# Kernel optimization log

Hardware: AMD Instinct MI355X
Metric: run time of the kernel (lower is better)

The kernel has to match this reference:

```python
import jax, jax.numpy as jnp
import numpy as np


def _pairwise_l2(set1, set2):
    # set1: [B, N, C], set2: [B, M, C] -> [B, N, M] Euclidean distances.
    # Equivalent to ||a - b||_2 computed via the expanded quadratic form,
    # avoiding the O(B*N*M*C) broadcasted-difference intermediate.
    sq1 = jnp.sum(set1 * set1, axis=-1)  # [B, N]
    sq2 = jnp.sum(set2 * set2, axis=-1)  # [B, M]
    inner = jnp.einsum('bnc,bmc->bnm', set1, set2)  # [B, N, M]
    d2 = sq1[:, :, None] + sq2[:, None, :] - 2.0 * inner
    return jnp.sqrt(jnp.maximum(d2, 0.0))


def reference(set1, set2):
    # mode == Hausdorff.average
    if set1.ndim == 2:
        set1 = set1[None]
    if set2.ndim == 2:
        set2 = set2[None]
    distances = _pairwise_l2(set1, set2)  # [B, N, M]
    term_1 = jnp.mean(jnp.min(distances, axis=2), axis=1)  # [B]
    term_2 = jnp.mean(jnp.min(distances, axis=1), axis=1)  # [B]
    res = term_1 + term_2
    if res.shape[0] == 1:
        res = jnp.squeeze(res, axis=0)
    return res


def setup_inputs() -> dict:
    key = jax.random.key(0)
    k1, k2 = jax.random.split(key)
    B, N, M, C = 8, 4096, 4096, 128
    set1 = jax.random.normal(k1, (B, N, C), dtype=jnp.float32)
    set2 = jax.random.normal(k2, (B, M, C), dtype=jnp.float32)
    return {"set1": set1, "set2": set2}
```

## Files before the change

### kernel.cpp

```cpp
#include <hip/hip_runtime.h>

#define B_ 8
#define N_ 4096
#define M_ 4096
#define C_ 128
#define BN_ (B_ * N_)
#define BM_ (B_ * M_)

typedef __attribute__((ext_vector_type(8))) short bf16x8;
typedef __attribute__((ext_vector_type(4))) float floatx4;
typedef __attribute__((ext_vector_type(8))) unsigned short ushort8;

__device__ __forceinline__ unsigned short f2bf(float x) {
    unsigned int u = __float_as_uint(x);
    u += 0x7FFFu + ((u >> 16) & 1u);
    return (unsigned short)(u >> 16);
}

__device__ __forceinline__ void gl2lds16(const void* g, void* l) {
    __builtin_amdgcn_global_load_lds(
        (const __attribute__((address_space(1))) void*)g,
        (__attribute__((address_space(3))) void*)l, 16, 0, 0);
}

__global__ __launch_bounds__(256) void prep_kernel(
    const float* __restrict__ S1, const float* __restrict__ S2,
    float* __restrict__ norms, unsigned short* __restrict__ bfA,
    unsigned short* __restrict__ bfB, float* __restrict__ out) {
    const int lane = threadIdx.x & 63;
    const int w    = threadIdx.x >> 6;
    const int gw   = blockIdx.x * 4 + w;
    const int r4   = lane >> 4;
    const int g4   = lane & 15;
    const int row  = gw * 4 + r4;

    const float* src = (row < BN_) ? S1 + (size_t)row * C_
                                   : S2 + (size_t)(row - BN_) * C_;
    float4 v0 = ((const float4*)src)[g4 * 2];
    float4 v1 = ((const float4*)src)[g4 * 2 + 1];

    float s = v0.x*v0.x + v0.y*v0.y + v0.z*v0.z + v0.w*v0.w
            + v1.x*v1.x + v1.y*v1.y + v1.z*v1.z + v1.w*v1.w;
    s += __shfl_xor(s, 1, 64);
    s += __shfl_xor(s, 2, 64);
    s += __shfl_xor(s, 4, 64);
    s += __shfl_xor(s, 8, 64);

    ushort8 o;
    o[0] = f2bf(v0.x); o[1] = f2bf(v0.y); o[2] = f2bf(v0.z); o[3] = f2bf(v0.w);
    o[4] = f2bf(v1.x); o[5] = f2bf(v1.y); o[6] = f2bf(v1.z); o[7] = f2bf(v1.w);

    unsigned short* dst = (row < BN_) ? bfA + (size_t)row * C_
                                      : bfB + (size_t)(row - BN_) * C_;
    *(ushort8*)&dst[(g4 ^ (row & 15)) * 8] = o;

    if (g4 == 0) norms[row] = -0.5f * s;
    if (blockIdx.x == 0 && threadIdx.x < B_) out[threadIdx.x] = 0.f;
}

__global__ __launch_bounds__(256, 2) void hausdorff_mfma(
    const unsigned short* __restrict__ Abf, const unsigned short* __restrict__ Bbf,
    const float* __restrict__ ahalf_g, const float* __restrict__ bhalf_g,
    float* __restrict__ rowpart, float* __restrict__ colpart) {

    __shared__ unsigned short B_lds[2][64 * 128];
    __shared__ float colmax_lds[2][1024];

    const int b     = blockIdx.z;
    const int row0  = blockIdx.x * 128;
    const int panel = blockIdx.y;
    const int tid   = threadIdx.x;
    const int lane  = tid & 63;
    const int w     = tid >> 6;
    const int lm    = lane & 15;
    const int quad  = lane >> 4;
    const int wrow  = (w >> 1) * 64;
    const int qc    = (w & 1) * 32;
    const int rh    = w >> 1;
    const int ch    = w & 1;

    const unsigned short* Aws = Abf + ((size_t)b * N_ + row0) * C_;
    const unsigned short* Bws = Bbf + ((size_t)b * M_ + (size_t)panel * 1024) * C_;
    const float* bhalf = bhalf_g + (size_t)b * M_ + panel * 1024;

    #pragma unroll
    for (int k = 0; k < 4; ++k) {
        const int off = w * 2048 + k * 512;
        gl2lds16(Aws + off + lane * 8,        &B_lds[0][off]);
        gl2lds16(Aws + 8192 + off + lane * 8, &B_lds[1][off]);
    }

    float ha[16];
    #pragma unroll
    for (int i = 0; i < 4; ++i) {
        float4 t = *(const float4*)&ahalf_g[(size_t)b * N_ + row0 + wrow + 16 * i + 4 * quad];
        ha[4*i+0] = t.x; ha[4*i+1] = t.y; ha[4*i+2] = t.z; ha[4*i+3] = t.w;
    }

    float rv[16];
    #pragma unroll
    for (int v = 0; v < 16; ++v) rv[v] = -1e30f;

    __syncthreads();

    bf16x8 af[4][4];
    {
        const unsigned short* Abuf = &B_lds[w >> 1][0];
        #pragma unroll
        for (int i = 0; i < 4; ++i)
            #pragma unroll
            for (int c = 0; c < 4; ++c)
                af[i][c] = *(const bf16x8*)
                    &Abuf[(16 * i + lm) * 128 + (((c * 4 + quad) ^ lm) * 8)];
    }

    __syncthreads();

    #pragma unroll
    for (int k = 0; k < 4; ++k) {
        const int off = w * 2048 + k * 512;
        gl2lds16(Bws + off + lane * 8, &B_lds[0][off]);
    }

    for (int it = 0; it < 16; ++it) {
        const int cur = it & 1;
        __syncthreads();

        if (it < 15) {
            const unsigned short* Bt = Bws + (size_t)(it + 1) * 64 * C_;
            #pragma unroll
            for (int k = 0; k < 4; ++k) {
                const int off = w * 2048 + k * 512;
                gl2lds16(Bt + off + lane * 8, &B_lds[cur ^ 1][off]);
            }
        }
        const float hb0 = bhalf[it * 64 + qc + lm];
        const float hb1 = bhalf[it * 64 + qc + 16 + lm];

        bf16x8 bf[2][4];
        #pragma unroll
        for (int j = 0; j < 2; ++j)
            #pragma unroll
            for (int c = 0; c < 4; ++c)
                bf[j][c] = *(const bf16x8*)
                    &B_lds[cur][(qc + 16 * j + lm) * 128 + (((c * 4 + quad) ^ lm) * 8)];

        floatx4 acc[4][2];
        #pragma unroll
        for (int i = 0; i < 4; ++i)
            #pragma unroll
            for (int r = 0; r < 4; ++r) {
                acc[i][0][r] = ha[4 * i + r] + hb0;
                acc[i][1][r] = ha[4 * i + r] + hb1;
            }
        #pragma unroll
        for (int c = 0; c < 4; ++c)
            #pragma unroll
            for (int i = 0; i < 4; ++i)
                #pragma unroll
                for (int j = 0; j < 2; ++j)
                    acc[i][j] = __builtin_amdgcn_mfma_f32_16x16x32_bf16(
                        af[i][c], bf[j][c], acc[i][j], 0, 0, 0);

        float cv0a = -1e30f, cv0b = -1e30f, cv1a = -1e30f, cv1b = -1e30f;
        #pragma unroll
        for (int i = 0; i < 4; ++i) {
            #pragma unroll
            for (int r = 0; r < 4; ++r)
                rv[4 * i + r] = fmaxf(rv[4 * i + r],
                                      fmaxf(acc[i][0][r], acc[i][1][r]));
            float m0 = fmaxf(fmaxf(acc[i][0][0], acc[i][0][1]),
                             fmaxf(acc[i][0][2], acc[i][0][3]));
            float m1 = fmaxf(fmaxf(acc[i][1][0], acc[i][1][1]),
                             fmaxf(acc[i][1][2], acc[i][1][3]));
            if (i & 1) { cv0b = fmaxf(cv0b, m0); cv1b = fmaxf(cv1b, m1); }
            else       { cv0a = fmaxf(cv0a, m0); cv1a = fmaxf(cv1a, m1); }
        }
        float cv0 = fmaxf(cv0a, cv0b), cv1 = fmaxf(cv1a, cv1b);
        cv0 = fmaxf(cv0, __shfl_xor(cv0, 16, 64));
        cv0 = fmaxf(cv0, __shfl_xor(cv0, 32, 64));
        cv1 = fmaxf(cv1, __shfl_xor(cv1, 16, 64));
        cv1 = fmaxf(cv1, __shfl_xor(cv1, 32, 64));
        if (quad == 0) {
            const int c0 = it * 64 + qc + lm;
            colmax_lds[rh][c0]      = cv0;
            colmax_lds[rh][c0 + 16] = cv1;
        }
    }

    float* rowmax_lds = (float*)&B_lds[0][0];
    #pragma unroll
    for (int s = 1; s < 16; s <<= 1)
        #pragma unroll
        for (int v = 0; v < 16; ++v)
            rv[v] = fmaxf(rv[v], __shfl_xor(rv[v], s, 64));
    if (lm == 0) {
        #pragma unroll
        for (int v = 0; v < 16; ++v)
            rowmax_lds[ch * 128 + wrow + 16 * (v >> 2) + 4 * quad + (v & 3)] = rv[v];
    }

    __syncthreads();

    #pragma unroll
    for (int k = 0; k < 4; ++k) {
        const int c = tid + 256 * k;
        colpart[((size_t)blockIdx.x * B_ + b) * M_ + (size_t)panel * 1024 + c] =
            fmaxf(colmax_lds[0][c], colmax_lds[1][c]);
    }
    if (tid < 128)
        rowpart[((size_t)panel * B_ + b) * N_ + row0 + tid] =
            fmaxf(rowmax_lds[tid], rowmax_lds[128 + tid]);
}

__global__ __launch_bounds__(256) void hausdorff_reduce(
    const float* __restrict__ rowpart, const float* __restrict__ colpart,
    float* __restrict__ out) {
    __shared__ float ws4[4];
    const int b    = blockIdx.x >> 3;
    const int part = blockIdx.x & 7;
    const int base = part * 512;
    float s = 0.f;
    for (int i = base + (int)threadIdx.x; i < base + 512; i += 256) {
        float ra = fmaxf(rowpart[((size_t)0 * B_ + b) * N_ + i],
                         rowpart[((size_t)1 * B_ + b) * N_ + i]);
        float rb = fmaxf(rowpart[((size_t)2 * B_ + b) * N_ + i],
                         rowpart[((size_t)3 * B_ + b) * N_ + i]);
        float rm = fmaxf(ra, rb);
        float ca = -1e30f, cb = -1e30f;
        #pragma unroll
        for (int x = 0; x < 32; x += 2) {
            ca = fmaxf(ca, colpart[((size_t)x * B_ + b) * M_ + i]);
            cb = fmaxf(cb, colpart[((size_t)(x + 1) * B_ + b) * M_ + i]);
        }
        float cm = fmaxf(ca, cb);
        s += sqrtf(fmaxf(-2.f * rm, 0.f)) * (1.f / N_)
           + sqrtf(fmaxf(-2.f * cm, 0.f)) * (1.f / M_);
    }
    #pragma unroll
    for (int off = 32; off > 0; off >>= 1) s += __shfl_down(s, off, 64);
    if ((threadIdx.x & 63) == 0) ws4[threadIdx.x >> 6] = s;
    __syncthreads();
    if (threadIdx.x == 0)
        atomicAdd(&out[b], ws4[0] + ws4[1] + ws4[2] + ws4[3]);
}

extern "C" void kernel_launch(void* const* d_in, const int* in_sizes, int n_in,
                              void* d_out, int out_size, void* d_ws, size_t ws_size,
                              hipStream_t stream) {
    const float* s1 = (const float*)d_in[0];
    const float* s2 = (const float*)d_in[1];
    float* out = (float*)d_out;

    float* norms         = (float*)d_ws;
    unsigned short* bfA  = (unsigned short*)(norms + BN_ + BM_);
    unsigned short* bfB  = bfA + (size_t)BN_ * C_;
    float* rowpart       = (float*)(bfB + (size_t)BM_ * C_);
    float* colpart       = rowpart + (size_t)4 * B_ * N_;

    prep_kernel<<<(BN_ + BM_) / 16, 256, 0, stream>>>(
        s1, s2, norms, bfA, bfB, out);

    dim3 grid(N_ / 128, M_ / 1024, B_);
    hausdorff_mfma<<<grid, 256, 0, stream>>>(
        bfA, bfB, norms, norms + BN_, rowpart, colpart);

    hausdorff_reduce<<<B_ * 8, 256, 0, stream>>>(rowpart, colpart, out);
}
```

Measured before the change: 123.7 us.

## Enlarge block row tile to 256 so each wave covers all 64 columns

Each block now handles 256 rows of set1, with each wave owning 64 rows and all 64 columns of every B tile, instead of a 2x2 split over 128 rows. A fragments are loaded straight from global memory into registers, bypassing LDS and two barriers. Row maxima are written directly to global memory. This halves the grid and the number of column-partial slabs the reduce kernel reads. The aim is more MFMA work per B tile loaded into LDS and less staging overhead, at the cost of 16 accumulators per wave (more register pressure) and half as many blocks.

```diff
diff --git a/kernel.cpp b/kernel.cpp
--- a/kernel.cpp
+++ b/kernel.cpp
@@ -64,31 +64,30 @@
     float* __restrict__ rowpart, float* __restrict__ colpart) {
 
     __shared__ unsigned short B_lds[2][64 * 128];
-    __shared__ float colmax_lds[2][1024];
+    __shared__ float colmax_lds[4][1024];
 
     const int b     = blockIdx.z;
-    const int row0  = blockIdx.x * 128;
+    const int x     = blockIdx.x;
     const int panel = blockIdx.y;
+    const int row0  = x * 256;
     const int tid   = threadIdx.x;
     const int lane  = tid & 63;
     const int w     = tid >> 6;
     const int lm    = lane & 15;
     const int quad  = lane >> 4;
-    const int wrow  = (w >> 1) * 64;
-    const int qc    = (w & 1) * 32;
-    const int rh    = w >> 1;
-    const int ch    = w & 1;
-
-    const unsigned short* Aws = Abf + ((size_t)b * N_ + row0) * C_;
+    const int wrow  = w * 64;
+
+    const unsigned short* Aws = Abf + ((size_t)b * N_ + row0 + wrow) * C_;
     const unsigned short* Bws = Bbf + ((size_t)b * M_ + (size_t)panel * 1024) * C_;
     const float* bhalf = bhalf_g + (size_t)b * M_ + panel * 1024;
 
-    #pragma unroll
-    for (int k = 0; k < 4; ++k) {
-        const int off = w * 2048 + k * 512;
-        gl2lds16(Aws + off + lane * 8,        &B_lds[0][off]);
-        gl2lds16(Aws + 8192 + off + lane * 8, &B_lds[1][off]);
-    }
+    bf16x8 af[4][4];
+    #pragma unroll
+    for (int i = 0; i < 4; ++i)
+        #pragma unroll
+        for (int c = 0; c < 4; ++c)
+            af[i][c] = *(const bf16x8*)
+                &Aws[(16 * i + lm) * 128 + (((c * 4 + quad) ^ lm) * 8)];
 
     float ha[16];
     #pragma unroll
@@ -100,21 +99,6 @@
     float rv[16];
     #pragma unroll
     for (int v = 0; v < 16; ++v) rv[v] = -1e30f;
-
-    __syncthreads();
-
-    bf16x8 af[4][4];
-    {
-        const unsigned short* Abuf = &B_lds[w >> 1][0];
-        #pragma unroll
-        for (int i = 0; i < 4; ++i)
-            #pragma unroll
-            for (int c = 0; c < 4; ++c)
-                af[i][c] = *(const bf16x8*)
-                    &Abuf[(16 * i + lm) * 128 + (((c * 4 + quad) ^ lm) * 8)];
-    }
-
-    __syncthreads();
 
     #pragma unroll
     for (int k = 0; k < 4; ++k) {
@@ -134,61 +118,68 @@
                 gl2lds16(Bt + off + lane * 8, &B_lds[cur ^ 1][off]);
             }
         }
-        const float hb0 = bhalf[it * 64 + qc + lm];
-        const float hb1 = bhalf[it * 64 + qc + 16 + lm];
-
-        bf16x8 bf[2][4];
-        #pragma unroll
-        for (int j = 0; j < 2; ++j)
+
+        float hb[4];
+        #pragma unroll
+        for (int j = 0; j < 4; ++j)
+            hb[j] = bhalf[it * 64 + 16 * j + lm];
+
+        floatx4 acc[4][4];
+        #pragma unroll
+        for (int i = 0; i < 4; ++i)
+            #pragma unroll
+            for (int j = 0; j < 4; ++j)
+                #pragma unroll
+                for (int r = 0; r < 4; ++r)
+                    acc[i][j][r] = ha[4 * i + r] + hb[j];
+
+        #pragma unroll
+        for (int h = 0; h < 2; ++h) {
+            bf16x8 bfr[2][4];
+            #pragma unroll
+            for (int j2 = 0; j2 < 2; ++j2)
+                #pragma unroll
+                for (int c = 0; c < 4; ++c)
+                    bfr[j2][c] = *(const bf16x8*)
+                        &B_lds[cur][(16 * (2 * h + j2) + lm) * 128 +
+                                    (((c * 4 + quad) ^ lm) * 8)];
             #pragma unroll
             for (int c = 0; c < 4; ++c)
-                bf[j][c] = *(const bf16x8*)
-                    &B_lds[cur][(qc + 16 * j + lm) * 128 + (((c * 4 + quad) ^ lm) * 8)];
-
-        floatx4 acc[4][2];
+                #pragma unroll
+                for (int i = 0; i < 4; ++i)
+                    #pragma unroll
+                    for (int j2 = 0; j2 < 2; ++j2)
+                        acc[i][2 * h + j2] = __builtin_amdgcn_mfma_f32_16x16x32_bf16(
+                            af[i][c], bfr[j2][c], acc[i][2 * h + j2], 0, 0, 0);
+        }
+
         #pragma unroll
         for (int i = 0; i < 4; ++i)
             #pragma unroll
             for (int r = 0; r < 4; ++r) {
-                acc[i][0][r] = ha[4 * i + r] + hb0;
-                acc[i][1][r] = ha[4 * i + r] + hb1;
+                float m01 = fmaxf(acc[i][0][r], acc[i][1][r]);
+                float m23 = fmaxf(acc[i][2][r], acc[i][3][r]);
+                rv[4 * i + r] = fmaxf(rv[4 * i + r], fmaxf(m01, m23));
             }
-        #pragma unroll
-        for (int c = 0; c < 4; ++c)
-            #pragma unroll
-            for (int i = 0; i < 4; ++i)
-                #pragma unroll
-                for (int j = 0; j < 2; ++j)
-                    acc[i][j] = __builtin_amdgcn_mfma_f32_16x16x32_bf16(
-                        af[i][c], bf[j][c], acc[i][j], 0, 0, 0);
-
-        float cv0a = -1e30f, cv0b = -1e30f, cv1a = -1e30f, cv1b = -1e30f;
-        #pragma unroll
-        for (int i = 0; i < 4; ++i) {
-            #pragma unroll
-            for (int r = 0; r < 4; ++r)
-                rv[4 * i + r] = fmaxf(rv[4 * i + r],
-                                      fmaxf(acc[i][0][r], acc[i][1][r]));
-            float m0 = fmaxf(fmaxf(acc[i][0][0], acc[i][0][1]),
-                             fmaxf(acc[i][0][2], acc[i][0][3]));
-            float m1 = fmaxf(fmaxf(acc[i][1][0], acc[i][1][1]),
-                             fmaxf(acc[i][1][2], acc[i][1][3]));
-            if (i & 1) { cv0b = fmaxf(cv0b, m0); cv1b = fmaxf(cv1b, m1); }
-            else       { cv0a = fmaxf(cv0a, m0); cv1a = fmaxf(cv1a, m1); }
-        }
-        float cv0 = fmaxf(cv0a, cv0b), cv1 = fmaxf(cv1a, cv1b);
-        cv0 = fmaxf(cv0, __shfl_xor(cv0, 16, 64));
-        cv0 = fmaxf(cv0, __shfl_xor(cv0, 32, 64));
-        cv1 = fmaxf(cv1, __shfl_xor(cv1, 16, 64));
-        cv1 = fmaxf(cv1, __shfl_xor(cv1, 32, 64));
-        if (quad == 0) {
-            const int c0 = it * 64 + qc + lm;
-            colmax_lds[rh][c0]      = cv0;
-            colmax_lds[rh][c0 + 16] = cv1;
-        }
-    }
-
-    float* rowmax_lds = (float*)&B_lds[0][0];
+
+        #pragma unroll
+        for (int j = 0; j < 4; ++j) {
+            float t0 = fmaxf(fmaxf(acc[0][j][0], acc[0][j][1]),
+                             fmaxf(acc[0][j][2], acc[0][j][3]));
+            float t1 = fmaxf(fmaxf(acc[1][j][0], acc[1][j][1]),
+                             fmaxf(acc[1][j][2], acc[1][j][3]));
+            float t2 = fmaxf(fmaxf(acc[2][j][0], acc[2][j][1]),
+                             fmaxf(acc[2][j][2], acc[2][j][3]));
+            float t3 = fmaxf(fmaxf(acc[3][j][0], acc[3][j][1]),
+                             fmaxf(acc[3][j][2], acc[3][j][3]));
+            float cv = fmaxf(fmaxf(t0, t1), fmaxf(t2, t3));
+            cv = fmaxf(cv, __shfl_xor(cv, 16, 64));
+            cv = fmaxf(cv, __shfl_xor(cv, 32, 64));
+            if (quad == 0)
+                colmax_lds[w][it * 64 + 16 * j + lm] = cv;
+        }
+    }
+
     #pragma unroll
     for (int s = 1; s < 16; s <<= 1)
         #pragma unroll
@@ -197,20 +188,25 @@
     if (lm == 0) {
         #pragma unroll
         for (int v = 0; v < 16; ++v)
-            rowmax_lds[ch * 128 + wrow + 16 * (v >> 2) + 4 * quad + (v & 3)] = rv[v];
+            rowpart[((size_t)panel * B_ + b) * N_ + row0 + wrow +
+                    16 * (v >> 2) + 4 * quad + (v & 3)] = rv[v];
     }
 
     __syncthreads();
 
-    #pragma unroll
-    for (int k = 0; k < 4; ++k) {
-        const int c = tid + 256 * k;
-        colpart[((size_t)blockIdx.x * B_ + b) * M_ + (size_t)panel * 1024 + c] =
-            fmaxf(colmax_lds[0][c], colmax_lds[1][c]);
-    }
-    if (tid < 128)
-        rowpart[((size_t)panel * B_ + b) * N_ + row0 + tid] =
-            fmaxf(rowmax_lds[tid], rowmax_lds[128 + tid]);
+    {
+        const int c = tid * 4;
+        float4 a0 = *(const float4*)&colmax_lds[0][c];
+        float4 a1 = *(const float4*)&colmax_lds[1][c];
+        float4 a2 = *(const float4*)&colmax_lds[2][c];
+        float4 a3 = *(const float4*)&colmax_lds[3][c];
+        float4 r;
+        r.x = fmaxf(fmaxf(a0.x, a1.x), fmaxf(a2.x, a3.x));
+        r.y = fmaxf(fmaxf(a0.y, a1.y), fmaxf(a2.y, a3.y));
+        r.z = fmaxf(fmaxf(a0.z, a1.z), fmaxf(a2.z, a3.z));
+        r.w = fmaxf(fmaxf(a0.w, a1.w), fmaxf(a2.w, a3.w));
+        *(float4*)&colpart[((size_t)x * B_ + b) * M_ + (size_t)panel * 1024 + c] = r;
+    }
 }
 
 __global__ __launch_bounds__(256) void hausdorff_reduce(
@@ -229,9 +225,9 @@
         float rm = fmaxf(ra, rb);
         float ca = -1e30f, cb = -1e30f;
         #pragma unroll
-        for (int x = 0; x < 32; x += 2) {
-            ca = fmaxf(ca, colpart[((size_t)x * B_ + b) * M_ + i]);
-            cb = fmaxf(cb, colpart[((size_t)(x + 1) * B_ + b) * M_ + i]);
+        for (int xx = 0; xx < 16; xx += 2) {
+            ca = fmaxf(ca, colpart[((size_t)xx * B_ + b) * M_ + i]);
+            cb = fmaxf(cb, colpart[((size_t)(xx + 1) * B_ + b) * M_ + i]);
         }
         float cm = fmaxf(ca, cb);
         s += sqrtf(fmaxf(-2.f * rm, 0.f)) * (1.f / N_)
@@ -261,7 +257,7 @@
     prep_kernel<<<(BN_ + BM_) / 16, 256, 0, stream>>>(
         s1, s2, norms, bfA, bfB, out);
 
-    dim3 grid(N_ / 128, M_ / 1024, B_);
+    dim3 grid(N_ / 256, M_ / 1024, B_);
     hausdorff_mfma<<<grid, 256, 0, stream>>>(
         bfA, bfB, norms, norms + BN_, rowpart, colpart);
 
```

New measurement: 121.4 us. About the same (-1.9%).
